# Performance work log

Measured on AMD Instinct MI355X. Metric: run time of the kernel, lower is better.

Reference implementation:

```python
import jax, jax.numpy as jnp
import numpy as np

B, N, T, D, O = 8, 1024, 12, 64, 64

def setup_inputs() -> dict:
    key = jax.random.key(0)
    k1, k2, k3 = jax.random.split(key, 3)
    x = jax.random.normal(k1, (B, N, T, D), dtype=jnp.float32)
    # row-normalized random adjacency (dense mask, as in the torch module)
    adj = jax.random.uniform(k2, (N, N), dtype=jnp.float32)
    norm_adj = adj / jnp.sum(adj, axis=-1, keepdims=True)
    theta_w = jax.random.normal(k3, (D, O), dtype=jnp.float32) / np.sqrt(D)
    return {"x": x, "norm_adj": norm_adj, "theta_w": theta_w}

def reference(x, norm_adj, theta_w):
    b, n, t, d = x.shape
    # [B, N, T, D] -> [B*T, N, D]
    xr = jnp.transpose(x, (0, 2, 1, 3)).reshape(b * t, n, d)
    # spatial attention scores [B*T, N, N]
    scores = jnp.einsum('gnd,gmd->gnm', xr, xr) / jnp.sqrt(jnp.float32(d))
    attn = jax.nn.softmax(scores, axis=-1)
    # adjacency-masked attention, then aggregate and project
    agg = jnp.einsum('gnm,gmd->gnd', norm_adj[None, :, :] * attn, xr)
    out = jnp.einsum('gnd,do->gno', agg, theta_w)
    # [B*T, N, O] -> [B, N, T, O], relu
    out = jnp.transpose(out.reshape(b, t, n, -1), (0, 2, 1, 3))
    return jax.nn.relu(out)
```

## Files before the change

kernel.cpp:

```cpp
#include <hip/hip_runtime.h>


#define NB    8
#define NT    12
#define NNODE 1024
#define ND    64
#define XROW  768
#define NG    96

typedef __bf16 bf16x8 __attribute__((ext_vector_type(8)));
typedef __bf16 bf16x4 __attribute__((ext_vector_type(4)));
typedef float  floatx4 __attribute__((ext_vector_type(4)));

#define MFMA(a,b,c) __builtin_amdgcn_mfma_f32_16x16x32_bf16((a),(b),(c),0,0,0)

#define QSCALE 0.18033688011112042f

#define KSTRIDE 72
#define VSTRIDE 40
#define OFF_KHI 0
#define OFF_KLO 4608
#define OFF_WHI 9216
#define OFF_WLO 14336
#define BUFSZ   19456
#define SMEM8   (2 * BUFSZ)
#define PSTRIDE 36
#define AGSTRIDE 68
#define OFF_VHI 9216
#define OFF_VLO 14336
#define OFF_P   19456
#define SMEM_FB (19456 + 128*PSTRIDE*4)

#define WXHI  0
#define WXLO  6291456
#define WVPHI 12582912
#define WVPLO 18874368
#define WS_BYTES 50348032ULL

struct bfpair { __bf16 h, l; };

__device__ __forceinline__ bfpair split1(float f) {
    bfpair r;
    __bf16 hb = (__bf16)f;
    float hf = __builtin_bit_cast(float,
                   (unsigned)__builtin_bit_cast(unsigned short, hb) << 16);
    r.h = hb;
    r.l = (__bf16)(f - hf);
    return r;
}

__global__ void __launch_bounds__(256)
presplit(const float* __restrict__ x, const float* __restrict__ theta,
         __bf16* __restrict__ ws)
{
    __shared__ __align__(16) float T[64 * 68];
    __shared__ __align__(16) float Wt[64 * 68];
    const int tid  = threadIdx.x;
    const int lane = tid & 63;
    const int wave = tid >> 6;
    const int l16  = lane & 15;
    const int quad = lane >> 4;
    const int bx   = blockIdx.x;
    const int g    = bx >> 4;
    const int nblk = bx & 15;
    const int bb   = g / NT;
    const int tt   = g - bb * NT;
    const int n0   = nblk * 64;

    __bf16* Xhi  = ws + WXHI  + (size_t)g * 65536;
    __bf16* Xlo  = ws + WXLO  + (size_t)g * 65536;
    __bf16* WPhi = ws + WVPHI + (size_t)g * 65536;
    __bf16* WPlo = ws + WVPLO + (size_t)g * 65536;
    const float* xg = x + (size_t)bb * (NNODE * XROW) + (size_t)tt * ND;

    #pragma unroll
    for (int i = 0; i < 4; ++i) {
        int chunk = i * 256 + tid;
        int n  = chunk >> 4;
        int c4 = (chunk & 15) * 4;
        floatx4 f = *(const floatx4*)(xg + (size_t)(n0 + n) * XROW + c4);
        *(floatx4*)(T + n * 68 + c4) = f;
        bf16x4 h, l;
        #pragma unroll
        for (int j = 0; j < 4; ++j) {
            bfpair p = split1(f[j]); h[j] = p.h; l[j] = p.l;
        }
        *(bf16x4*)(Xhi + (size_t)(n0 + n) * 64 + c4) = h;
        *(bf16x4*)(Xlo + (size_t)(n0 + n) * 64 + c4) = l;
    }
    __syncthreads();

    {
        bf16x8 tah[2], tal[2];
        #pragma unroll
        for (int ks = 0; ks < 2; ++ks)
            #pragma unroll
            for (int j = 0; j < 8; ++j) {
                bfpair p = split1(T[(wave*16 + l16)*68 + ks*32 + quad*8 + j]);
                tah[ks][j] = p.h; tal[ks][j] = p.l;
            }
        const floatx4 vz = {0.f, 0.f, 0.f, 0.f};
        #pragma unroll
        for (int ot = 0; ot < 4; ++ot) {
            bf16x8 thb[2], tlb[2];
            #pragma unroll
            for (int ks = 0; ks < 2; ++ks)
                #pragma unroll
                for (int j = 0; j < 8; ++j) {
                    bfpair p = split1(theta[(size_t)(ks*32 + quad*8 + j) * ND
                                            + ot*16 + l16]);
                    thb[ks][j] = p.h; tlb[ks][j] = p.l;
                }
            floatx4 Wc = vz;
            #pragma unroll
            for (int ks = 0; ks < 2; ++ks) {
                Wc = MFMA(tah[ks], thb[ks], Wc);
                Wc = MFMA(tal[ks], thb[ks], Wc);
                Wc = MFMA(tah[ks], tlb[ks], Wc);
            }
            #pragma unroll
            for (int r = 0; r < 4; ++r)
                Wt[(wave*16 + quad*4 + r)*68 + ot*16 + l16] = Wc[r];
        }
    }
    __syncthreads();

    {
        const int o  = tid >> 2;
        const int nc = (tid & 3) * 16;
        const int tb = nc & 32;
        bf16x8 h0, l0, h1, l1;
        #pragma unroll
        for (int j = 0; j < 8; ++j) {
            int c0 = (nc & 31) + j;
            int k0 = ((c0 & 7) >> 2) * 16 + (c0 >> 3) * 4 + (c0 & 3);
            bfpair p = split1(Wt[(tb + k0) * 68 + o]);
            h0[j] = p.h; l0[j] = p.l;
            int c1 = (nc & 31) + 8 + j;
            int k1 = ((c1 & 7) >> 2) * 16 + (c1 >> 3) * 4 + (c1 & 3);
            bfpair q = split1(Wt[(tb + k1) * 68 + o]);
            h1[j] = q.h; l1[j] = q.l;
        }
        __bf16* dsth = WPhi + (size_t)o * NNODE + n0 + nc;
        __bf16* dstl = WPlo + (size_t)o * NNODE + n0 + nc;
        *(bf16x8*)dsth = h0; *(bf16x8*)(dsth + 8) = h1;
        *(bf16x8*)dstl = l0; *(bf16x8*)(dstl + 8) = l1;
    }
}

__global__ void __launch_bounds__(256, 3)
spattn10(const __bf16* __restrict__ ws, const float* __restrict__ adj,
         float* __restrict__ out)
{
    __shared__ __align__(16) char smem[SMEM8];

    const int tid  = threadIdx.x;
    const int wave = tid >> 6;
    const int lane = tid & 63;
    const int l16  = lane & 15;
    const int quad = lane >> 4;

    const int bx   = blockIdx.x;
    const int g    = bx % NG;
    const int rblk = bx / NG;
    const int bb   = g / NT;
    const int tt   = g - bb * NT;
    const int row0 = rblk * 128;

    const __bf16* xh  = ws + WXHI  + (size_t)g * 65536;
    const __bf16* xl  = ws + WXLO  + (size_t)g * 65536;
    const __bf16* wph = ws + WVPHI + (size_t)g * 65536;
    const __bf16* wpl = ws + WVPLO + (size_t)g * 65536;

    bf16x8 qhi[2][2], qlo[2][2];
    #pragma unroll
    for (int mt = 0; mt < 2; ++mt) {
        const __bf16* q0 = xh + (size_t)(row0 + wave*32 + mt*16 + l16) * 64 + quad*8;
        const __bf16* q1 = xl + (size_t)(row0 + wave*32 + mt*16 + l16) * 64 + quad*8;
        #pragma unroll
        for (int ks = 0; ks < 2; ++ks) {
            qhi[mt][ks] = *(const bf16x8*)(q0 + ks*32);
            qlo[mt][ks] = *(const bf16x8*)(q1 + ks*32);
        }
    }

    const floatx4 vzero = {0.f, 0.f, 0.f, 0.f};
    floatx4 acc[2][4];
    #pragma unroll
    for (int mt = 0; mt < 2; ++mt)
        #pragma unroll
        for (int dt = 0; dt < 4; ++dt)
            acc[mt][dt] = vzero;
    float lpart[2] = {0.f, 0.f};

    const int skey = tid >> 3;
    const int sd0  = (tid & 7) * 8;
    const int svd  = tid >> 2;
    const int svk0 = (tid & 3) * 8;

    bf16x8 kh, kl, wh, wl;
    kh = *(const bf16x8*)(xh  + (size_t)skey * 64 + sd0);
    kl = *(const bf16x8*)(xl  + (size_t)skey * 64 + sd0);
    wh = *(const bf16x8*)(wph + (size_t)svd * NNODE + svk0);
    wl = *(const bf16x8*)(wpl + (size_t)svd * NNODE + svk0);
    {
        char* b0 = smem;
        *(bf16x8*)((__bf16*)(b0 + OFF_KHI) + skey*KSTRIDE + sd0) = kh;
        *(bf16x8*)((__bf16*)(b0 + OFF_KLO) + skey*KSTRIDE + sd0) = kl;
        *(bf16x8*)((__bf16*)(b0 + OFF_WHI) + svd*VSTRIDE + svk0) = wh;
        *(bf16x8*)((__bf16*)(b0 + OFF_WLO) + svd*VSTRIDE + svk0) = wl;
    }
    kh = *(const bf16x8*)(xh  + (size_t)(32 + skey) * 64 + sd0);
    kl = *(const bf16x8*)(xl  + (size_t)(32 + skey) * 64 + sd0);
    wh = *(const bf16x8*)(wph + (size_t)svd * NNODE + 32 + svk0);
    wl = *(const bf16x8*)(wpl + (size_t)svd * NNODE + 32 + svk0);

    int cur = 0;
    for (int ct = 0; ct < 32; ++ct) {
        const int key0 = ct * 32;
        __syncthreads();
        if (ct < 31) {
            char* wb = smem + (cur ^ 1) * BUFSZ;
            *(bf16x8*)((__bf16*)(wb + OFF_KHI) + skey*KSTRIDE + sd0) = kh;
            *(bf16x8*)((__bf16*)(wb + OFF_KLO) + skey*KSTRIDE + sd0) = kl;
            *(bf16x8*)((__bf16*)(wb + OFF_WHI) + svd*VSTRIDE + svk0) = wh;
            *(bf16x8*)((__bf16*)(wb + OFF_WLO) + svd*VSTRIDE + svk0) = wl;
        }
        if (ct < 30) {
            const int nk = key0 + 64;
            kh = *(const bf16x8*)(xh  + (size_t)(nk + skey) * 64 + sd0);
            kl = *(const bf16x8*)(xl  + (size_t)(nk + skey) * 64 + sd0);
            wh = *(const bf16x8*)(wph + (size_t)svd * NNODE + nk + svk0);
            wl = *(const bf16x8*)(wpl + (size_t)svd * NNODE + nk + svk0);
        }
        floatx4 av[2][2];
        #pragma unroll
        for (int mt = 0; mt < 2; ++mt)
            #pragma unroll
            for (int nt = 0; nt < 2; ++nt)
                av[mt][nt] = *(const floatx4*)(adj
                    + (size_t)(row0 + wave*32 + mt*16 + l16) * NNODE
                    + key0 + nt*16 + quad*4);

        char* rb = smem + cur * BUFSZ;
        __bf16* Khi = (__bf16*)(rb + OFF_KHI);
        __bf16* Klo = (__bf16*)(rb + OFF_KLO);
        __bf16* Whi = (__bf16*)(rb + OFF_WHI);
        __bf16* Wlo = (__bf16*)(rb + OFF_WLO);

        floatx4 S[2][2] = {{vzero, vzero}, {vzero, vzero}};
        __builtin_amdgcn_s_setprio(1);
        #pragma unroll
        for (int ks = 0; ks < 2; ++ks) {
            #pragma unroll
            for (int nt = 0; nt < 2; ++nt) {
                bf16x8 ah = *(const bf16x8*)(Khi + (nt*16 + l16)*KSTRIDE + ks*32 + quad*8);
                bf16x8 al = *(const bf16x8*)(Klo + (nt*16 + l16)*KSTRIDE + ks*32 + quad*8);
                #pragma unroll
                for (int mt = 0; mt < 2; ++mt) {
                    S[mt][nt] = MFMA(ah, qhi[mt][ks], S[mt][nt]);
                    S[mt][nt] = MFMA(ah, qlo[mt][ks], S[mt][nt]);
                    S[mt][nt] = MFMA(al, qhi[mt][ks], S[mt][nt]);
                }
            }
        }
        __builtin_amdgcn_s_setprio(0);

        bf16x8 pah[2], pal[2];
        #pragma unroll
        for (int mt = 0; mt < 2; ++mt)
            #pragma unroll
            for (int nt = 0; nt < 2; ++nt)
                #pragma unroll
                for (int r = 0; r < 4; ++r) {
                    float w = __builtin_amdgcn_exp2f(S[mt][nt][r] * QSCALE);
                    lpart[mt] += w;
                    bfpair pp = split1(av[mt][nt][r] * w);
                    pah[mt][nt*4 + r] = pp.h;
                    pal[mt][nt*4 + r] = pp.l;
                }

        __builtin_amdgcn_s_setprio(1);
        #pragma unroll
        for (int dt = 0; dt < 4; ++dt) {
            bf16x8 wvh = *(const bf16x8*)(Whi + (dt*16 + l16)*VSTRIDE + quad*8);
            bf16x8 wvl = *(const bf16x8*)(Wlo + (dt*16 + l16)*VSTRIDE + quad*8);
            #pragma unroll
            for (int mt = 0; mt < 2; ++mt) {
                acc[mt][dt] = MFMA(pah[mt], wvh, acc[mt][dt]);
                acc[mt][dt] = MFMA(pal[mt], wvh, acc[mt][dt]);
                acc[mt][dt] = MFMA(pah[mt], wvl, acc[mt][dt]);
            }
        }
        __builtin_amdgcn_s_setprio(0);
        cur ^= 1;
    }

    float linv[2][4];
    #pragma unroll
    for (int mt = 0; mt < 2; ++mt) {
        float lv = lpart[mt];
        lv += __shfl_xor(lv, 16);
        lv += __shfl_xor(lv, 32);
        #pragma unroll
        for (int r = 0; r < 4; ++r)
            linv[mt][r] = 1.0f / __shfl(lv, quad*4 + r);
    }

    float* obase = out + (size_t)bb * (NNODE * XROW) + tt * ND;
    #pragma unroll
    for (int mt = 0; mt < 2; ++mt)
        #pragma unroll
        for (int dt = 0; dt < 4; ++dt)
            #pragma unroll
            for (int r = 0; r < 4; ++r) {
                float v = acc[mt][dt][r] * linv[mt][r];
                obase[(size_t)(row0 + wave*32 + mt*16 + quad*4 + r) * XROW + dt*16 + l16]
                    = v > 0.f ? v : 0.f;
            }
}

__global__ void __launch_bounds__(256, 2)
spattn_fb(const float* __restrict__ x, const float* __restrict__ adj,
          const float* __restrict__ theta, float* __restrict__ out)
{
    __shared__ __align__(16) char smem[SMEM_FB];
    __bf16* Khi = (__bf16*)(smem + OFF_KHI);
    __bf16* Klo = (__bf16*)(smem + OFF_KLO);
    __bf16* Vhi = (__bf16*)(smem + OFF_VHI);
    __bf16* Vlo = (__bf16*)(smem + OFF_VLO);
    float*  Pm  = (float*)(smem + OFF_P);

    const int tid  = threadIdx.x;
    const int wave = tid >> 6;
    const int lane = tid & 63;
    const int l16  = lane & 15;
    const int quad = lane >> 4;

    const int bx   = blockIdx.x;
    const int g    = bx >> 3;
    const int rblk = bx & 7;
    const int bb   = g / NT;
    const int tt   = g - bb * NT;
    const int row0 = rblk * 128;

    const float* xbase = x + (size_t)bb * (NNODE * XROW) + tt * ND;

    bf16x8 qhi[2][2], qlo[2][2];
    #pragma unroll
    for (int mt = 0; mt < 2; ++mt) {
        const float* qsrc = xbase + (size_t)(row0 + wave*32 + mt*16 + l16) * XROW;
        #pragma unroll
        for (int ks = 0; ks < 2; ++ks) {
            floatx4 f0 = *(const floatx4*)(qsrc + ks*32 + quad*8);
            floatx4 f1 = *(const floatx4*)(qsrc + ks*32 + quad*8 + 4);
            #pragma unroll
            for (int i = 0; i < 4; ++i) {
                bfpair p0 = split1(f0[i]*QSCALE);
                qhi[mt][ks][i]   = p0.h; qlo[mt][ks][i]   = p0.l;
                bfpair p1 = split1(f1[i]*QSCALE);
                qhi[mt][ks][4+i] = p1.h; qlo[mt][ks][4+i] = p1.l;
            }
        }
    }

    const floatx4 vzero = {0.f, 0.f, 0.f, 0.f};
    floatx4 acc[2][4];
    #pragma unroll
    for (int mt = 0; mt < 2; ++mt)
        #pragma unroll
        for (int dt = 0; dt < 4; ++dt)
            acc[mt][dt] = vzero;
    float lpart[2][4] = {{0.f,0.f,0.f,0.f},{0.f,0.f,0.f,0.f}};

    const int skey = tid >> 3;
    const int sd0  = (tid & 7) * 8;
    const int svd  = tid >> 2;
    const int svk0 = (tid & 3) * 8;
    floatx4 kf0, kf1;
    float vf[8];

    {
        const float* ksrc = xbase + (size_t)skey * XROW + sd0;
        kf0 = *(const floatx4*)ksrc;
        kf1 = *(const floatx4*)(ksrc + 4);
        const float* vsrc = xbase + (size_t)svk0 * XROW + svd;
        #pragma unroll
        for (int i = 0; i < 8; ++i) vf[i] = vsrc[i * XROW];
    }

    for (int ct = 0; ct < 32; ++ct) {
        const int key0 = ct * 32;
        __syncthreads();
        {
            bf16x8 h, l;
            #pragma unroll
            for (int i = 0; i < 4; ++i) {
                bfpair p0 = split1(kf0[i]); h[i]   = p0.h; l[i]   = p0.l;
                bfpair p1 = split1(kf1[i]); h[4+i] = p1.h; l[4+i] = p1.l;
            }
            *(bf16x8*)(Khi + skey*KSTRIDE + sd0) = h;
            *(bf16x8*)(Klo + skey*KSTRIDE + sd0) = l;
            bf16x8 vh, vl;
            #pragma unroll
            for (int i = 0; i < 8; ++i) {
                bfpair p = split1(vf[i]); vh[i] = p.h; vl[i] = p.l;
            }
            *(bf16x8*)(Vhi + svd*VSTRIDE + svk0) = vh;
            *(bf16x8*)(Vlo + svd*VSTRIDE + svk0) = vl;
        }
        __syncthreads();
        if (ct < 31) {
            const int nk = key0 + 32;
            const float* ksrc = xbase + (size_t)(nk + skey) * XROW + sd0;
            kf0 = *(const floatx4*)ksrc;
            kf1 = *(const floatx4*)(ksrc + 4);
            const float* vsrc = xbase + (size_t)(nk + svk0) * XROW + svd;
            #pragma unroll
            for (int i = 0; i < 8; ++i) vf[i] = vsrc[i * XROW];
        }
        float av[2][2][4];
        #pragma unroll
        for (int mt = 0; mt < 2; ++mt)
            #pragma unroll
            for (int nt = 0; nt < 2; ++nt)
                #pragma unroll
                for (int r = 0; r < 4; ++r)
                    av[mt][nt][r] = adj[(size_t)(row0 + wave*32 + mt*16 + quad*4 + r) * NNODE
                                        + key0 + nt*16 + l16];

        floatx4 S[2][2] = {{vzero, vzero}, {vzero, vzero}};
        #pragma unroll
        for (int ks = 0; ks < 2; ++ks) {
            #pragma unroll
            for (int nt = 0; nt < 2; ++nt) {
                bf16x8 bh = *(const bf16x8*)(Khi + (nt*16 + l16)*KSTRIDE + ks*32 + quad*8);
                bf16x8 bl = *(const bf16x8*)(Klo + (nt*16 + l16)*KSTRIDE + ks*32 + quad*8);
                #pragma unroll
                for (int mt = 0; mt < 2; ++mt) {
                    S[mt][nt] = MFMA(qhi[mt][ks], bh, S[mt][nt]);
                    S[mt][nt] = MFMA(qlo[mt][ks], bh, S[mt][nt]);
                    S[mt][nt] = MFMA(qhi[mt][ks], bl, S[mt][nt]);
                }
            }
        }
        #pragma unroll
        for (int mt = 0; mt < 2; ++mt)
            #pragma unroll
            for (int nt = 0; nt < 2; ++nt)
                #pragma unroll
                for (int r = 0; r < 4; ++r) {
                    float w = __builtin_amdgcn_exp2f(S[mt][nt][r]);
                    lpart[mt][r] += w;
                    Pm[(wave*32 + mt*16 + quad*4 + r)*PSTRIDE + nt*16 + l16] = av[mt][nt][r] * w;
                }
        bf16x8 pah[2], pal[2];
        #pragma unroll
        for (int mt = 0; mt < 2; ++mt) {
            const float* pp = Pm + (wave*32 + mt*16 + l16)*PSTRIDE + quad*8;
            floatx4 p0 = *(const floatx4*)pp;
            floatx4 p1 = *(const floatx4*)(pp + 4);
            #pragma unroll
            for (int i = 0; i < 4; ++i) {
                bfpair q0 = split1(p0[i]); pah[mt][i]   = q0.h; pal[mt][i]   = q0.l;
                bfpair q1 = split1(p1[i]); pah[mt][4+i] = q1.h; pal[mt][4+i] = q1.l;
            }
        }
        #pragma unroll
        for (int dt = 0; dt < 4; ++dt) {
            bf16x8 vh = *(const bf16x8*)(Vhi + (dt*16 + l16)*VSTRIDE + quad*8);
            bf16x8 vl = *(const bf16x8*)(Vlo + (dt*16 + l16)*VSTRIDE + quad*8);
            #pragma unroll
            for (int mt = 0; mt < 2; ++mt) {
                acc[mt][dt] = MFMA(pah[mt], vh, acc[mt][dt]);
                acc[mt][dt] = MFMA(pal[mt], vh, acc[mt][dt]);
                acc[mt][dt] = MFMA(pah[mt], vl, acc[mt][dt]);
            }
        }
    }

    float linv[2][4];
    #pragma unroll
    for (int mt = 0; mt < 2; ++mt)
        #pragma unroll
        for (int r = 0; r < 4; ++r) {
            float lv = lpart[mt][r];
            lv += __shfl_xor(lv, 1);
            lv += __shfl_xor(lv, 2);
            lv += __shfl_xor(lv, 4);
            lv += __shfl_xor(lv, 8);
            linv[mt][r] = 1.0f / lv;
        }

    __syncthreads();
    float* AG = (float*)smem;
    #pragma unroll
    for (int mt = 0; mt < 2; ++mt)
        #pragma unroll
        for (int dt = 0; dt < 4; ++dt)
            #pragma unroll
            for (int r = 0; r < 4; ++r)
                AG[(wave*32 + mt*16 + quad*4 + r)*AGSTRIDE + dt*16 + l16]
                    = acc[mt][dt][r] * linv[mt][r];

    bf16x8 th[4][2], tl[4][2];
    #pragma unroll
    for (int ot = 0; ot < 4; ++ot)
        #pragma unroll
        for (int ks = 0; ks < 2; ++ks)
            #pragma unroll
            for (int j = 0; j < 8; ++j) {
                float tv = theta[(ks*32 + quad*8 + j)*ND + ot*16 + l16];
                bfpair p = split1(tv);
                th[ot][ks][j] = p.h; tl[ot][ks][j] = p.l;
            }

    floatx4 oacc[2][4];
    #pragma unroll
    for (int mt = 0; mt < 2; ++mt)
        #pragma unroll
        for (int ot = 0; ot < 4; ++ot)
            oacc[mt][ot] = vzero;
    __syncthreads();
    #pragma unroll
    for (int ks = 0; ks < 2; ++ks) {
        bf16x8 ah[2], al[2];
        #pragma unroll
        for (int mt = 0; mt < 2; ++mt) {
            const float* ap = AG + (wave*32 + mt*16 + l16)*AGSTRIDE + ks*32 + quad*8;
            floatx4 a0 = *(const floatx4*)ap;
            floatx4 a1 = *(const floatx4*)(ap + 4);
            #pragma unroll
            for (int i = 0; i < 4; ++i) {
                bfpair q0 = split1(a0[i]); ah[mt][i]   = q0.h; al[mt][i]   = q0.l;
                bfpair q1 = split1(a1[i]); ah[mt][4+i] = q1.h; al[mt][4+i] = q1.l;
            }
        }
        #pragma unroll
        for (int ot = 0; ot < 4; ++ot)
            #pragma unroll
            for (int mt = 0; mt < 2; ++mt) {
                oacc[mt][ot] = MFMA(ah[mt], th[ot][ks], oacc[mt][ot]);
                oacc[mt][ot] = MFMA(al[mt], th[ot][ks], oacc[mt][ot]);
                oacc[mt][ot] = MFMA(ah[mt], tl[ot][ks], oacc[mt][ot]);
            }
    }

    float* obase = out + (size_t)bb * (NNODE * XROW) + tt * ND;
    #pragma unroll
    for (int mt = 0; mt < 2; ++mt)
        #pragma unroll
        for (int ot = 0; ot < 4; ++ot)
            #pragma unroll
            for (int r = 0; r < 4; ++r) {
                float v = oacc[mt][ot][r];
                obase[(size_t)(row0 + wave*32 + mt*16 + quad*4 + r) * XROW + ot*16 + l16]
                    = v > 0.f ? v : 0.f;
            }
}

extern "C" void kernel_launch(void* const* d_in, const int* in_sizes, int n_in,
                              void* d_out, int out_size, void* d_ws, size_t ws_size,
                              hipStream_t stream) {
    (void)in_sizes; (void)n_in; (void)out_size;
    const float* x     = (const float*)d_in[0];
    const float* adj   = (const float*)d_in[1];
    const float* theta = (const float*)d_in[2];
    float* out = (float*)d_out;
    if (d_ws != nullptr && ws_size >= WS_BYTES) {
        __bf16* ws = (__bf16*)d_ws;
        presplit<<<dim3(1536), dim3(256), 0, stream>>>(x, theta, ws);
        spattn10<<<dim3(768), dim3(256), 0, stream>>>(ws, adj, out);
    } else {
        spattn_fb<<<dim3(768), dim3(256), 0, stream>>>(x, adj, theta, out);
    }
}
```

Before: 167.4 us.

## Stage K and V tiles with direct global-to-LDS loads and XOR-swizzled layout

The main attention kernel now copies each K hi/lo and projected-V hi/lo tile straight from global memory into LDS with 16-byte global_load_lds instructions. This replaces the old path that loaded into registers and then stored to padded LDS. The padded strides are replaced by an XOR-swizzled unpadded layout so MFMA operand reads avoid bank conflicts, which shrinks the double buffer. The goal is to cut register pressure and the VGPR-to-LDS store instructions. In exchange, prefetch depth drops from two tiles ahead to one, and correctness now depends on the async loads being complete before the barrier.

```diff
diff --git a/kernel.cpp b/kernel.cpp
--- a/kernel.cpp
+++ b/kernel.cpp
@@ -16,16 +16,18 @@
 
 #define QSCALE 0.18033688011112042f
 
+#define OKH 0
+#define OKL 4096
+#define OWH 8192
+#define OWL 12288
+#define BUF2 16384
+#define SMEM12 (2 * BUF2)
 #define KSTRIDE 72
 #define VSTRIDE 40
+#define PSTRIDE 36
+#define AGSTRIDE 68
 #define OFF_KHI 0
 #define OFF_KLO 4608
-#define OFF_WHI 9216
-#define OFF_WLO 14336
-#define BUFSZ   19456
-#define SMEM8   (2 * BUFSZ)
-#define PSTRIDE 36
-#define AGSTRIDE 68
 #define OFF_VHI 9216
 #define OFF_VLO 14336
 #define OFF_P   19456
@@ -47,6 +49,12 @@
     r.h = hb;
     r.l = (__bf16)(f - hf);
     return r;
+}
+
+__device__ __forceinline__ void gld16(const __bf16* g, char* l) {
+    __builtin_amdgcn_global_load_lds(
+        (const __attribute__((address_space(1))) void*)g,
+        (__attribute__((address_space(3))) void*)l, 16, 0, 0);
 }
 
 __global__ void __launch_bounds__(256)
@@ -149,10 +157,10 @@
 }
 
 __global__ void __launch_bounds__(256, 3)
-spattn10(const __bf16* __restrict__ ws, const float* __restrict__ adj,
+spattn12(const __bf16* __restrict__ ws, const float* __restrict__ adj,
          float* __restrict__ out)
 {
-    __shared__ __align__(16) char smem[SMEM8];
+    __shared__ __align__(16) char smem[SMEM12];
 
     const int tid  = threadIdx.x;
     const int wave = tid >> 6;
@@ -172,6 +180,11 @@
     const __bf16* wph = ws + WVPHI + (size_t)g * 65536;
     const __bf16* wpl = ws + WVPLO + (size_t)g * 65536;
 
+    const int kc   = (lane & 7) ^ (lane >> 3);
+    const int krow = (wave << 3) + (lane >> 3);
+    const int wo   = ((wave << 3) + (lane >> 3)) * 2 + ((kc & 4) >> 2);
+    const int wko  = (kc & 3) * 8;
+
     bf16x8 qhi[2][2], qlo[2][2];
     #pragma unroll
     for (int mt = 0; mt < 2; ++mt) {
@@ -193,45 +206,25 @@
             acc[mt][dt] = vzero;
     float lpart[2] = {0.f, 0.f};
 
-    const int skey = tid >> 3;
-    const int sd0  = (tid & 7) * 8;
-    const int svd  = tid >> 2;
-    const int svk0 = (tid & 3) * 8;
-
-    bf16x8 kh, kl, wh, wl;
-    kh = *(const bf16x8*)(xh  + (size_t)skey * 64 + sd0);
-    kl = *(const bf16x8*)(xl  + (size_t)skey * 64 + sd0);
-    wh = *(const bf16x8*)(wph + (size_t)svd * NNODE + svk0);
-    wl = *(const bf16x8*)(wpl + (size_t)svd * NNODE + svk0);
     {
         char* b0 = smem;
-        *(bf16x8*)((__bf16*)(b0 + OFF_KHI) + skey*KSTRIDE + sd0) = kh;
-        *(bf16x8*)((__bf16*)(b0 + OFF_KLO) + skey*KSTRIDE + sd0) = kl;
-        *(bf16x8*)((__bf16*)(b0 + OFF_WHI) + svd*VSTRIDE + svk0) = wh;
-        *(bf16x8*)((__bf16*)(b0 + OFF_WLO) + svd*VSTRIDE + svk0) = wl;
-    }
-    kh = *(const bf16x8*)(xh  + (size_t)(32 + skey) * 64 + sd0);
-    kl = *(const bf16x8*)(xl  + (size_t)(32 + skey) * 64 + sd0);
-    wh = *(const bf16x8*)(wph + (size_t)svd * NNODE + 32 + svk0);
-    wl = *(const bf16x8*)(wpl + (size_t)svd * NNODE + 32 + svk0);
+        gld16(xh  + (size_t)krow * 64 + kc*8,          b0 + OKH + wave*1024);
+        gld16(xl  + (size_t)krow * 64 + kc*8,          b0 + OKL + wave*1024);
+        gld16(wph + (size_t)wo * NNODE + wko,          b0 + OWH + wave*1024);
+        gld16(wpl + (size_t)wo * NNODE + wko,          b0 + OWL + wave*1024);
+    }
 
     int cur = 0;
     for (int ct = 0; ct < 32; ++ct) {
         const int key0 = ct * 32;
         __syncthreads();
         if (ct < 31) {
-            char* wb = smem + (cur ^ 1) * BUFSZ;
-            *(bf16x8*)((__bf16*)(wb + OFF_KHI) + skey*KSTRIDE + sd0) = kh;
-            *(bf16x8*)((__bf16*)(wb + OFF_KLO) + skey*KSTRIDE + sd0) = kl;
-            *(bf16x8*)((__bf16*)(wb + OFF_WHI) + svd*VSTRIDE + svk0) = wh;
-            *(bf16x8*)((__bf16*)(wb + OFF_WLO) + svd*VSTRIDE + svk0) = wl;
-        }
-        if (ct < 30) {
-            const int nk = key0 + 64;
-            kh = *(const bf16x8*)(xh  + (size_t)(nk + skey) * 64 + sd0);
-            kl = *(const bf16x8*)(xl  + (size_t)(nk + skey) * 64 + sd0);
-            wh = *(const bf16x8*)(wph + (size_t)svd * NNODE + nk + svk0);
-            wl = *(const bf16x8*)(wpl + (size_t)svd * NNODE + nk + svk0);
+            const int nk = key0 + 32;
+            char* wb = smem + (cur ^ 1) * BUF2;
+            gld16(xh  + (size_t)(nk + krow) * 64 + kc*8, wb + OKH + wave*1024);
+            gld16(xl  + (size_t)(nk + krow) * 64 + kc*8, wb + OKL + wave*1024);
+            gld16(wph + (size_t)wo * NNODE + nk + wko,   wb + OWH + wave*1024);
+            gld16(wpl + (size_t)wo * NNODE + nk + wko,   wb + OWL + wave*1024);
         }
         floatx4 av[2][2];
         #pragma unroll
@@ -242,11 +235,11 @@
                     + (size_t)(row0 + wave*32 + mt*16 + l16) * NNODE
                     + key0 + nt*16 + quad*4);
 
-        char* rb = smem + cur * BUFSZ;
-        __bf16* Khi = (__bf16*)(rb + OFF_KHI);
-        __bf16* Klo = (__bf16*)(rb + OFF_KLO);
-        __bf16* Whi = (__bf16*)(rb + OFF_WHI);
-        __bf16* Wlo = (__bf16*)(rb + OFF_WLO);
+        char* rb = smem + cur * BUF2;
+        __bf16* Khi = (__bf16*)(rb + OKH);
+        __bf16* Klo = (__bf16*)(rb + OKL);
+        __bf16* Whi = (__bf16*)(rb + OWH);
+        __bf16* Wlo = (__bf16*)(rb + OWL);
 
         floatx4 S[2][2] = {{vzero, vzero}, {vzero, vzero}};
         __builtin_amdgcn_s_setprio(1);
@@ -254,8 +247,9 @@
         for (int ks = 0; ks < 2; ++ks) {
             #pragma unroll
             for (int nt = 0; nt < 2; ++nt) {
-                bf16x8 ah = *(const bf16x8*)(Khi + (nt*16 + l16)*KSTRIDE + ks*32 + quad*8);
-                bf16x8 al = *(const bf16x8*)(Klo + (nt*16 + l16)*KSTRIDE + ks*32 + quad*8);
+                const int kch = (((ks*4 + quad) ^ (l16 & 7))) * 8;
+                bf16x8 ah = *(const bf16x8*)(Khi + (nt*16 + l16)*64 + kch);
+                bf16x8 al = *(const bf16x8*)(Klo + (nt*16 + l16)*64 + kch);
                 #pragma unroll
                 for (int mt = 0; mt < 2; ++mt) {
                     S[mt][nt] = MFMA(ah, qhi[mt][ks], S[mt][nt]);
@@ -283,8 +277,10 @@
         __builtin_amdgcn_s_setprio(1);
         #pragma unroll
         for (int dt = 0; dt < 4; ++dt) {
-            bf16x8 wvh = *(const bf16x8*)(Whi + (dt*16 + l16)*VSTRIDE + quad*8);
-            bf16x8 wvl = *(const bf16x8*)(Wlo + (dt*16 + l16)*VSTRIDE + quad*8);
+            const int wmr = dt*8 + (l16 >> 1);
+            const int wch = ((((l16 & 1)*4 + quad) ^ ((l16 >> 1) & 7))) * 8;
+            bf16x8 wvh = *(const bf16x8*)(Whi + wmr*64 + wch);
+            bf16x8 wvl = *(const bf16x8*)(Wlo + wmr*64 + wch);
             #pragma unroll
             for (int mt = 0; mt < 2; ++mt) {
                 acc[mt][dt] = MFMA(pah[mt], wvh, acc[mt][dt]);
@@ -570,7 +566,7 @@
     if (d_ws != nullptr && ws_size >= WS_BYTES) {
         __bf16* ws = (__bf16*)d_ws;
         presplit<<<dim3(1536), dim3(256), 0, stream>>>(x, theta, ws);
-        spattn10<<<dim3(768), dim3(256), 0, stream>>>(ws, adj, out);
+        spattn12<<<dim3(768), dim3(256), 0, stream>>>(ws, adj, out);
     } else {
         spattn_fb<<<dim3(768), dim3(256), 0, stream>>>(x, adj, theta, out);
     }
```

New measurement: 166.4 us (median of 3 runs). Within noise of the previous version (-0.6%).
